# Performance work log

Measured on AMD Instinct MI355X. Metric: run time of the kernel, lower is better.

Reference implementation:

```python
import jax, jax.numpy as jnp
import numpy as np
from jax import lax

B, N = 8, 107136          # batch, anchors (248*216*2)
SCORE_THRESH = 0.05
PRE_MAX = 2048            # nms_pre_max_sizes[0]
POST_MAX = 128            # nms_post_max_sizes[0]
IOU_THRESH = 0.5
NUM_DIR_BINS = 2
DIR_OFFSET = 0.0
POST_CENTER_RANGE = np.array([0.0, -39.68, -5.0, 69.12, 39.68, 5.0], np.float32)


def setup_inputs() -> dict:
    key = jax.random.key(0)
    k1, k2, k3, k4, k5 = jax.random.split(key, 5)
    box_preds = jax.random.normal(k1, (B, N, 7), jnp.float32) * 0.3
    cls_preds = jax.random.normal(k2, (B, N, 2), jnp.float32) * 2.0
    dir_preds = jax.random.normal(k3, (B, N, 2), jnp.float32)
    # realistic KITTI car anchors: (x, y, z, w, l, h, r)
    xs = jax.random.uniform(k4, (B, N), jnp.float32, 0.0, 69.12)
    ys = jax.random.uniform(k5, (B, N), jnp.float32, -39.68, 39.68)
    zs = jnp.full((B, N), -1.0, jnp.float32)
    w = jnp.full((B, N), 1.6, jnp.float32)
    l = jnp.full((B, N), 3.9, jnp.float32)
    h = jnp.full((B, N), 1.56, jnp.float32)
    r = jnp.broadcast_to(jnp.where(jnp.arange(N) % 2 == 0, 0.0, np.pi / 2).astype(jnp.float32), (B, N))
    anchors = jnp.stack([xs, ys, zs, w, l, h, r], axis=-1)
    return {"box_preds": box_preds, "cls_preds": cls_preds, "dir_preds": dir_preds, "anchors": anchors}


def _decode(bp, an):
    # GroundBox3dCoder.decode_torch (second/pointpillars), code order (x,y,z,w,l,h,r)
    xa, ya, za, wa, la, ha, ra = [an[..., i] for i in range(7)]
    xt, yt, zt, wt, lt, ht, rt = [bp[..., i] for i in range(7)]
    za = za + ha * 0.5
    diag = jnp.sqrt(la * la + wa * wa)
    xg = xt * diag + xa
    yg = yt * diag + ya
    zg = zt * ha + za
    lg = jnp.exp(lt) * la
    wg = jnp.exp(wt) * wa
    hg = jnp.exp(ht) * ha
    rg = rt + ra
    zg = zg - hg * 0.5
    return jnp.stack([xg, yg, zg, wg, lg, hg, rg], axis=-1)


def _standup(boxes):
    # boxes: [K,7] decoded; rotated 2d rect -> axis-aligned standup box (x1,y1,x2,y2)
    x, y, w, l, r = boxes[:, 0], boxes[:, 1], boxes[:, 3], boxes[:, 4], boxes[:, 6]
    c, s = jnp.abs(jnp.cos(r)), jnp.abs(jnp.sin(r))
    hx = 0.5 * (w * c + l * s)
    hy = 0.5 * (w * s + l * c)
    return jnp.stack([x - hx, y - hy, x + hx, y + hy], axis=-1)


def _pairwise_iou(bb):
    # bb: [K,4] standup boxes
    x1, y1, x2, y2 = bb[:, 0], bb[:, 1], bb[:, 2], bb[:, 3]
    area = (x2 - x1) * (y2 - y1)
    ix = jnp.maximum(0.0, jnp.minimum(x2[:, None], x2[None, :]) - jnp.maximum(x1[:, None], x1[None, :]))
    iy = jnp.maximum(0.0, jnp.minimum(y2[:, None], y2[None, :]) - jnp.maximum(y1[:, None], y1[None, :]))
    inter = ix * iy
    return inter / jnp.maximum(area[:, None] + area[None, :] - inter, 1e-8)


def _greedy_nms(ious, valid):
    K = valid.shape[0]
    idxs = jnp.arange(K)
    def body(i, keep):
        sup = (ious[i] > IOU_THRESH) & (idxs > i) & keep[i]
        return keep & ~sup
    return lax.fori_loop(0, K, body, valid)


def _limit_period(val, offset, period):
    return val - jnp.floor(val / period + offset) * period


def _predict_one(boxes, scores, dir_labels):
    # boxes [N,7], scores [N], dir_labels [N] int32 (already sorted? no: raw)
    masked = jnp.where(scores >= SCORE_THRESH, scores, -jnp.inf)
    top_s, idx = lax.top_k(masked, PRE_MAX)           # sorted desc
    b = boxes[idx]                                    # [K,7]
    dl = dir_labels[idx]
    valid = jnp.isfinite(top_s)
    ious = _pairwise_iou(_standup(b))
    keep = _greedy_nms(lax.stop_gradient(ious), valid)
    kept = jnp.where(keep, top_s, -jnp.inf)
    sel_s, sel_i = lax.top_k(kept, POST_MAX)
    sel_b = b[sel_i]
    sel_dl = dl[sel_i].astype(sel_b.dtype)
    period = 2.0 * np.pi / NUM_DIR_BINS
    dir_rot = _limit_period(sel_b[:, 6] - DIR_OFFSET, 0.0, period)
    new_r = dir_rot + DIR_OFFSET + period * sel_dl
    sel_b = jnp.concatenate([sel_b[:, :6], new_r[:, None]], axis=-1)
    pcr = jnp.asarray(POST_CENTER_RANGE)
    in_range = jnp.all(sel_b[:, :3] >= pcr[:3], axis=1) & jnp.all(sel_b[:, :3] <= pcr[3:], axis=1)
    mask = jnp.isfinite(sel_s) & in_range
    out_s = jnp.where(mask, sel_s, 0.0)
    out_b = jnp.where(mask[:, None], sel_b, 0.0)
    labels = jnp.zeros((POST_MAX,), jnp.int32)  # single fg class -> label 0
    return out_b, out_s, labels, mask


def reference(box_preds, cls_preds, dir_preds, anchors):
    decoded = _decode(box_preds, anchors)                    # [B,N,7]
    scores = jax.nn.softmax(cls_preds, axis=-1)[..., 1]      # [B,N]
    dir_labels = jnp.argmax(dir_preds, axis=-1).astype(jnp.int32)
    return jax.vmap(_predict_one)(decoded, scores, dir_labels)
```

## Files before the change

kernel.cpp:

```cpp
#include <hip/hip_runtime.h>
#include <stdint.h>

#define NB 8
#define NN 107136
#define TOTAL (NB * NN)
#define NPAIR (NN / 2)
#define PRE 2048
#define POST 128
#define CAP 4096
#define HBINS 128
#define KEYBASE 0xBF00u
#define SCORE_TH 0.05f
#define SH_BPB 53

static constexpr size_t OFF_SCORES = 0;
static constexpr size_t SZ_SCORES  = (size_t)TOTAL * 4;
static constexpr size_t OFF_HIST   = OFF_SCORES + SZ_SCORES;
static constexpr size_t SZ_HIST    = (size_t)NB * HBINS * 4;
static constexpr size_t OFF_CNT    = OFF_HIST + SZ_HIST;
static constexpr size_t SZ_CNT     = (size_t)NB * 64 * 4;
static constexpr size_t OFF_T      = OFF_CNT + SZ_CNT;
static constexpr size_t OFF_CAND   = OFF_T + 256;
static constexpr size_t SZ_CAND    = (size_t)NB * CAP * 8;
static constexpr size_t OFF_SELS   = OFF_CAND + SZ_CAND;
static constexpr size_t OFF_SELI   = OFF_SELS + (size_t)NB * PRE * 4;
static constexpr size_t OFF_SELB   = OFF_SELI + (size_t)NB * PRE * 4;
static constexpr size_t OFF_SBB    = OFF_SELB + (size_t)NB * PRE * 7 * 4;
static constexpr size_t OFF_SAR    = OFF_SBB + (size_t)NB * PRE * 4 * 4;
static constexpr size_t OFF_MASK   = OFF_SAR + (size_t)NB * PRE * 4;
static constexpr size_t SZ_MASK    = (size_t)NB * PRE * 32 * 8;


__global__ void k_zero(uint32_t* p, int nwords) {
    int g = blockIdx.x * 256 + threadIdx.x;
    if (g < nwords) p[g] = 0u;
}

__global__ void __launch_bounds__(256) k_scoreshist(const float* __restrict__ cls,
                                                    float* __restrict__ scores,
                                                    uint32_t* __restrict__ hist) {
    int b = blockIdx.y;
    __shared__ uint32_t lh[HBINS];
    int t = threadIdx.x;
    if (t < HBINS) lh[t] = 0u;
    __syncthreads();
    const float4* cp = (const float4*)cls + (size_t)b * NPAIR;
    float2* sp = (float2*)scores + (size_t)b * NPAIR;
#pragma unroll
    for (int k = 0; k < 4; k++) {
        int p = blockIdx.x * 1024 + k * 256 + t;
        if (p < NPAIR) {
            float4 c = cp[p];
            float m0 = fmaxf(c.x, c.y);
            float s0 = __fdiv_rn(expf(__fsub_rn(c.y, m0)),
                                 __fadd_rn(expf(__fsub_rn(c.x, m0)), expf(__fsub_rn(c.y, m0))));
            float m1 = fmaxf(c.z, c.w);
            float s1 = __fdiv_rn(expf(__fsub_rn(c.w, m1)),
                                 __fadd_rn(expf(__fsub_rn(c.z, m1)), expf(__fsub_rn(c.w, m1))));
            sp[p] = make_float2(s0, s1);
            if (s0 >= 0.5f) {
                uint32_t bin = ((__float_as_uint(s0) >> 16) | 0x8000u) - KEYBASE;
                if (bin > 127u) bin = 127u;
                atomicAdd(&lh[bin], 1u);
            }
            if (s1 >= 0.5f) {
                uint32_t bin = ((__float_as_uint(s1) >> 16) | 0x8000u) - KEYBASE;
                if (bin > 127u) bin = 127u;
                atomicAdd(&lh[bin], 1u);
            }
        }
    }
    __syncthreads();
    if (t < HBINS && lh[t]) atomicAdd(&hist[b * HBINS + t], lh[t]);
}

__global__ void __launch_bounds__(64) k_findT(const uint32_t* __restrict__ hist,
                                              uint32_t* __restrict__ Tout) {
    int b = blockIdx.x, t = threadIdx.x;
    const uint32_t* h = hist + b * HBINS;
    uint32_t h0 = h[2 * t], h1 = h[2 * t + 1];
    uint32_t v = h0 + h1;
    for (int off = 1; off < 64; off <<= 1) {
        uint32_t u = __shfl_down(v, off);
        if (t + off >= 64) u = 0u;
        v += u;
    }
    uint32_t total = __shfl(v, 0);
    int c = -1;
    if (v - h0 >= PRE) c = 2 * t + 1;
    else if (v >= PRE) c = 2 * t;
    for (int off = 32; off > 0; off >>= 1) c = max(c, __shfl_xor(c, off));
    if (t == 0) Tout[b] = (total >= PRE && c >= 0) ? (KEYBASE + (uint32_t)c) : 0u;
}

__global__ void __launch_bounds__(256) k_compact(const float* __restrict__ scores,
                                                 const uint32_t* __restrict__ T,
                                                 uint32_t* __restrict__ counts,
                                                 uint64_t* __restrict__ cand) {
    int g2 = blockIdx.x * 256 + threadIdx.x;
    int lane = threadIdx.x & 63, wid = threadIdx.x >> 6;
    float2 sv = ((const float2*)scores)[g2];
    int e0 = 2 * g2;
    int b = e0 / NN;
    uint32_t Tb = T[b];
    uint32_t key0 = __float_as_uint(sv.x) | 0x80000000u;
    uint32_t key1 = __float_as_uint(sv.y) | 0x80000000u;
    bool p0 = (sv.x >= SCORE_TH) && ((key0 >> 16) >= Tb);
    bool p1 = (sv.y >= SCORE_TH) && ((key1 >> 16) >= Tb);
    uint64_t bal0 = __ballot(p0), bal1 = __ballot(p1);
    uint32_t n0 = (uint32_t)__popcll(bal0);
    uint32_t wcnt = n0 + (uint32_t)__popcll(bal1);
    uint64_t below = (lane == 63) ? ~0ull >> 1 : ((1ull << lane) - 1ull);
    below = (1ull << lane) - 1ull;
    uint32_t off0 = (uint32_t)__popcll(bal0 & below);
    uint32_t off1 = n0 + (uint32_t)__popcll(bal1 & below);
    __shared__ uint32_t lcnt[2];
    __shared__ uint32_t gbase[2];
    __shared__ uint32_t wbase[4];
    int b0 = (blockIdx.x * 512) / NN;
    if (threadIdx.x < 2) lcnt[threadIdx.x] = 0u;
    __syncthreads();
    if (lane == 0 && wcnt) wbase[wid] = atomicAdd(&lcnt[b - b0], wcnt);
    __syncthreads();
    if (threadIdx.x < 2 && lcnt[threadIdx.x])
        gbase[threadIdx.x] = atomicAdd(&counts[(size_t)(b0 + threadIdx.x) * 64], lcnt[threadIdx.x]);
    __syncthreads();
    if (p0 | p1) {
        uint32_t base = gbase[b - b0] + wbase[wid];
        if (p0) {
            uint32_t slot = base + off0;
            if (slot < CAP)
                cand[(size_t)b * CAP + slot] =
                    ((uint64_t)key0 << 32) | (uint64_t)(0xFFFFFFFFu - (uint32_t)(e0 - b * NN));
        }
        if (p1) {
            uint32_t slot = base + off1;
            if (slot < CAP)
                cand[(size_t)b * CAP + slot] =
                    ((uint64_t)key1 << 32) | (uint64_t)(0xFFFFFFFFu - (uint32_t)(e0 + 1 - b * NN));
        }
    }
}

__global__ void __launch_bounds__(256) k_rank_decode(
        const uint64_t* __restrict__ cand, const uint32_t* __restrict__ counts,
        const float* __restrict__ box_preds, const float* __restrict__ anchors,
        float* __restrict__ selS, uint32_t* __restrict__ selI,
        float* __restrict__ selB, float* __restrict__ selBB, float* __restrict__ selA) {
    int b = blockIdx.y;
    int i = blockIdx.x * 256 + threadIdx.x;
    int m = (int)counts[(size_t)b * 64]; if (m > CAP) m = CAP;
    const uint64_t* cb = cand + (size_t)b * CAP;
    uint64_t mykey = (i < m) ? cb[i] : 0ull;
    __shared__ uint64_t tile[512];
    int rank = 0;
    for (int base = 0; base < m; base += 512) {
        int nt = min(512, m - base);
        for (int j = threadIdx.x; j < nt; j += 256) tile[j] = cb[base + j];
        __syncthreads();
        if (i < m) {
            int j = 0;
            for (; j + 8 <= nt; j += 8) {
#pragma unroll
                for (int u = 0; u < 8; u++) rank += (tile[j + u] > mykey) ? 1 : 0;
            }
            for (; j < nt; j++) rank += (tile[j] > mykey) ? 1 : 0;
        }
        __syncthreads();
    }
    if (i >= m || rank >= PRE) return;
    size_t o = (size_t)b * PRE + rank;
    uint32_t key = (uint32_t)(mykey >> 32);
    uint32_t idx = 0xFFFFFFFFu - (uint32_t)(mykey & 0xFFFFFFFFull);
    float score = __uint_as_float(key & 0x7FFFFFFFu);
    const float* bp = box_preds + ((size_t)b * NN + idx) * 7;
    const float* an = anchors + ((size_t)b * NN + idx) * 7;
    float xa = an[0], ya = an[1], za = an[2], wa = an[3], la = an[4], ha = an[5], ra = an[6];
    float xt = bp[0], yt = bp[1], zt = bp[2], wt = bp[3], lt = bp[4], ht = bp[5], rt = bp[6];
    float za2  = __fadd_rn(za, __fmul_rn(ha, 0.5f));
    float diag = sqrtf(__fadd_rn(__fmul_rn(la, la), __fmul_rn(wa, wa)));
    float xg = __fadd_rn(__fmul_rn(xt, diag), xa);
    float yg = __fadd_rn(__fmul_rn(yt, diag), ya);
    float zg = __fadd_rn(__fmul_rn(zt, ha), za2);
    float lg = __fmul_rn(expf(lt), la);
    float wg = __fmul_rn(expf(wt), wa);
    float hg = __fmul_rn(expf(ht), ha);
    float rg = __fadd_rn(rt, ra);
    zg = __fsub_rn(zg, __fmul_rn(hg, 0.5f));
    selS[o] = score; selI[o] = idx;
    selB[o * 7 + 0] = xg; selB[o * 7 + 1] = yg; selB[o * 7 + 2] = zg;
    selB[o * 7 + 3] = wg; selB[o * 7 + 4] = lg; selB[o * 7 + 5] = hg;
    selB[o * 7 + 6] = rg;
    float cc = fabsf(cosf(rg)), ss = fabsf(sinf(rg));
    float hx = __fmul_rn(0.5f, __fadd_rn(__fmul_rn(wg, cc), __fmul_rn(lg, ss)));
    float hy = __fmul_rn(0.5f, __fadd_rn(__fmul_rn(wg, ss), __fmul_rn(lg, cc)));
    float x1 = __fsub_rn(xg, hx), y1 = __fsub_rn(yg, hy);
    float x2 = __fadd_rn(xg, hx), y2 = __fadd_rn(yg, hy);
    selBB[o * 4 + 0] = x1; selBB[o * 4 + 1] = y1;
    selBB[o * 4 + 2] = x2; selBB[o * 4 + 3] = y2;
    selA[o] = __fmul_rn(__fsub_rn(x2, x1), __fsub_rn(y2, y1));
}

__global__ void __launch_bounds__(256) k_iou(const float* __restrict__ selBB,
                                             const float* __restrict__ selA,
                                             uint64_t* __restrict__ maskrows) {
    int b = blockIdx.y;
    int r0 = blockIdx.x * 64;
    __shared__ float sx1[PRE], sy1[PRE], sx2[PRE], sy2[PRE], sar[PRE];
    int t = threadIdx.x;
    for (int i = t; i < PRE; i += 256) {
        const float* p = selBB + ((size_t)b * PRE + i) * 4;
        sx1[i] = p[0]; sy1[i] = p[1]; sx2[i] = p[2]; sy2[i] = p[3];
        sar[i] = selA[(size_t)b * PRE + i];
    }
    __syncthreads();
    int w  = t & 31;
    int rl = t >> 5;
    int jbase = w * 64;
    float rx1[8], ry1[8], rx2[8], ry2[8], rar[8];
    int rows[8];
#pragma unroll
    for (int p = 0; p < 8; p++) {
        int i = r0 + rl * 8 + p;
        rows[p] = i;
        rx1[p] = sx1[i]; ry1[p] = sy1[i]; rx2[p] = sx2[i]; ry2[p] = sy2[i]; rar[p] = sar[i];
    }
    uint64_t bits[8] = {0, 0, 0, 0, 0, 0, 0, 0};
    for (int jj = 0; jj < 64; jj++) {
        int j = jbase + ((jj + w) & 63);
        float xj1 = sx1[j], yj1 = sy1[j], xj2 = sx2[j], yj2 = sy2[j], aj = sar[j];
#pragma unroll
        for (int p = 0; p < 8; p++) {
            float ix = fmaxf(0.f, __fsub_rn(fminf(rx2[p], xj2), fmaxf(rx1[p], xj1)));
            float iy = fmaxf(0.f, __fsub_rn(fminf(ry2[p], yj2), fmaxf(ry1[p], yj1)));
            float inter = __fmul_rn(ix, iy);
            float den = fmaxf(__fsub_rn(__fadd_rn(rar[p], aj), inter), 1e-8f);
            float iou = __fdiv_rn(inter, den);
            if (iou > 0.5f && j > rows[p]) bits[p] |= (1ull << (j - jbase));
        }
    }
#pragma unroll
    for (int p = 0; p < 8; p++)
        maskrows[((size_t)b * PRE + rows[p]) * 32 + w] = bits[p];
}

__global__ void __launch_bounds__(128) k_nms_final(
        const uint64_t* __restrict__ maskrows, const float* __restrict__ selS,
        const uint32_t* __restrict__ selI, const float* __restrict__ selB,
        const uint32_t* __restrict__ counts, const float* __restrict__ dir_preds,
        float* __restrict__ out) {
    int b = blockIdx.x;
    __shared__ int keptIdx[POST];
    __shared__ int keptCount;
    int t = threadIdx.x;
    int Mv = (int)counts[(size_t)b * 64]; if (Mv > PRE) Mv = PRE;
    if (t < 64) {
        uint64_t removed = 0ull;
        int kc = 0;
        const uint64_t* mb = maskrows + (size_t)b * PRE * 32;
        uint64_t pre[8];
#pragma unroll
        for (int d = 0; d < 8; d++)
            pre[d] = (t < 32 && d < Mv) ? mb[(size_t)d * 32 + t] : 0ull;
        for (int i = 0; i < Mv && kc < POST; i++) {
            uint64_t mrow = pre[i & 7];
            int nf = i + 8;
            pre[i & 7] = (t < 32 && nf < Mv) ? mb[(size_t)nf * 32 + t] : 0ull;
            uint64_t rw = __shfl(removed, i >> 6);
            if (!((rw >> (i & 63)) & 1ull)) {
                if (t == 0) keptIdx[kc] = i;
                kc++;
                removed |= mrow;
            }
        }
        if (t == 0) keptCount = kc;
    }
    __syncthreads();
    int kc = keptCount;
    size_t ob = (size_t)b * POST + t;
    float box[7] = {0.f, 0.f, 0.f, 0.f, 0.f, 0.f, 0.f};
    float sc = 0.f, mk = 0.f;
    if (t < kc) {
        int i = keptIdx[t];
        size_t o = (size_t)b * PRE + i;
        float s = selS[o];
        uint32_t idx = selI[o];
        const float* bx = selB + o * 7;
        float d0 = dir_preds[((size_t)b * NN + idx) * 2 + 0];
        float d1 = dir_preds[((size_t)b * NN + idx) * 2 + 1];
        float label = (d1 > d0) ? 1.0f : 0.0f;
        const float period = 3.14159265358979323846f;
        float r = bx[6];
        float dir_rot = __fsub_rn(r, __fmul_rn(floorf(__fdiv_rn(r, period)), period));
        float nr = __fadd_rn(dir_rot, __fmul_rn(period, label));
        float x = bx[0], y = bx[1], z = bx[2];
        bool in_range = (x >= 0.0f) && (y >= -39.68f) && (z >= -5.0f) &&
                        (x <= 69.12f) && (y <= 39.68f) && (z <= 5.0f);
        if (in_range) {
            box[0] = x; box[1] = y; box[2] = z;
            box[3] = bx[3]; box[4] = bx[4]; box[5] = bx[5]; box[6] = nr;
            sc = s; mk = 1.f;
        }
    }
    float* out_b = out;
    float* out_s = out + 7168;
    float* out_l = out + 8192;
    float* out_m = out + 9216;
    for (int c = 0; c < 7; c++) out_b[ob * 7 + c] = box[c];
    out_s[ob] = sc;
    out_l[ob] = 0.f;
    out_m[ob] = mk;
}

extern "C" void kernel_launch(void* const* d_in, const int* in_sizes, int n_in,
                              void* d_out, int out_size, void* d_ws, size_t ws_size,
                              hipStream_t stream) {
    const float* box_preds = (const float*)d_in[0];
    const float* cls_preds = (const float*)d_in[1];
    const float* dir_preds = (const float*)d_in[2];
    const float* anchors   = (const float*)d_in[3];
    float* out = (float*)d_out;
    char* ws = (char*)d_ws;

    float*    scores = (float*)(ws + OFF_SCORES);
    uint32_t* hist   = (uint32_t*)(ws + OFF_HIST);
    uint32_t* counts = (uint32_t*)(ws + OFF_CNT);
    uint32_t* T      = (uint32_t*)(ws + OFF_T);
    uint64_t* cand   = (uint64_t*)(ws + OFF_CAND);
    float*    selS   = (float*)(ws + OFF_SELS);
    uint32_t* selI   = (uint32_t*)(ws + OFF_SELI);
    float*    selB   = (float*)(ws + OFF_SELB);
    float*    selBB  = (float*)(ws + OFF_SBB);
    float*    selA   = (float*)(ws + OFF_SAR);
    uint64_t* maskrows = (uint64_t*)(ws + OFF_MASK);

    int zwords = (int)((SZ_HIST + SZ_CNT + 256) / 4);
    k_zero<<<(zwords + 255) / 256, 256, 0, stream>>>(hist, zwords);

    dim3 gSH(SH_BPB, NB);
    k_scoreshist<<<gSH, 256, 0, stream>>>(cls_preds, scores, hist);
    k_findT<<<NB, 64, 0, stream>>>(hist, T);
    k_compact<<<TOTAL / 512, 256, 0, stream>>>(scores, T, counts, cand);
    dim3 gRank(CAP / 256, NB);
    k_rank_decode<<<gRank, 256, 0, stream>>>(cand, counts, box_preds, anchors,
                                             selS, selI, selB, selBB, selA);
    dim3 gIou(PRE / 64, NB);
    k_iou<<<gIou, 256, 0, stream>>>(selBB, selA, maskrows);
    k_nms_final<<<NB, 128, 0, stream>>>(maskrows, selS, selI, selB, counts,
                                        dir_preds, out);
}
```

Before: 222.2 us.

## Drop zero kernel, rewrite rank with ballot counting, halve IoU rows per block

The score histogram now writes per-block partial histograms that k_findT reduces, so the global atomics and the separate zeroing kernel go away. k_findT also resets the candidate count and clears the candidate buffer. The rank kernel exits early for empty blocks and counts larger keys with wave ballots over keys read straight from global memory, replacing the shared-tile pairwise loop. The IoU kernel processes 4 rows per thread instead of 8, doubling the grid, and replaces the divide with a multiply-compare, which can flip a decision when inter/den is right at 0.5 under rounding.

```diff
diff --git a/kernel.cpp b/kernel.cpp
--- a/kernel.cpp
+++ b/kernel.cpp
@@ -16,7 +16,7 @@
 static constexpr size_t OFF_SCORES = 0;
 static constexpr size_t SZ_SCORES  = (size_t)TOTAL * 4;
 static constexpr size_t OFF_HIST   = OFF_SCORES + SZ_SCORES;
-static constexpr size_t SZ_HIST    = (size_t)NB * HBINS * 4;
+static constexpr size_t SZ_HIST    = (size_t)NB * SH_BPB * HBINS * 4;
 static constexpr size_t OFF_CNT    = OFF_HIST + SZ_HIST;
 static constexpr size_t SZ_CNT     = (size_t)NB * 64 * 4;
 static constexpr size_t OFF_T      = OFF_CNT + SZ_CNT;
@@ -31,14 +31,9 @@
 static constexpr size_t SZ_MASK    = (size_t)NB * PRE * 32 * 8;
 
 
-__global__ void k_zero(uint32_t* p, int nwords) {
-    int g = blockIdx.x * 256 + threadIdx.x;
-    if (g < nwords) p[g] = 0u;
-}
-
 __global__ void __launch_bounds__(256) k_scoreshist(const float* __restrict__ cls,
                                                     float* __restrict__ scores,
-                                                    uint32_t* __restrict__ hist) {
+                                                    uint32_t* __restrict__ hp) {
     int b = blockIdx.y;
     __shared__ uint32_t lh[HBINS];
     int t = threadIdx.x;
@@ -71,26 +66,42 @@
         }
     }
     __syncthreads();
-    if (t < HBINS && lh[t]) atomicAdd(&hist[b * HBINS + t], lh[t]);
-}
-
-__global__ void __launch_bounds__(64) k_findT(const uint32_t* __restrict__ hist,
-                                              uint32_t* __restrict__ Tout) {
+    if (t < HBINS) hp[((size_t)b * SH_BPB + blockIdx.x) * HBINS + t] = lh[t];
+}
+
+__global__ void __launch_bounds__(256) k_findT(const uint32_t* __restrict__ hp,
+                                               uint32_t* __restrict__ Tout,
+                                               uint32_t* __restrict__ counts,
+                                               uint64_t* __restrict__ cand) {
     int b = blockIdx.x, t = threadIdx.x;
-    const uint32_t* h = hist + b * HBINS;
-    uint32_t h0 = h[2 * t], h1 = h[2 * t + 1];
-    uint32_t v = h0 + h1;
-    for (int off = 1; off < 64; off <<= 1) {
-        uint32_t u = __shfl_down(v, off);
-        if (t + off >= 64) u = 0u;
-        v += u;
-    }
-    uint32_t total = __shfl(v, 0);
-    int c = -1;
-    if (v - h0 >= PRE) c = 2 * t + 1;
-    else if (v >= PRE) c = 2 * t;
-    for (int off = 32; off > 0; off >>= 1) c = max(c, __shfl_xor(c, off));
-    if (t == 0) Tout[b] = (total >= PRE && c >= 0) ? (KEYBASE + (uint32_t)c) : 0u;
+    __shared__ uint32_t hbin[HBINS];
+    if (t < HBINS) {
+        uint32_t s = 0;
+        for (int sg = 0; sg < SH_BPB; sg++)
+            s += hp[((size_t)b * SH_BPB + sg) * HBINS + t];
+        hbin[t] = s;
+    }
+    __syncthreads();
+    if (t < 64) {
+        uint32_t h0 = hbin[2 * t], h1 = hbin[2 * t + 1];
+        uint32_t v = h0 + h1;
+        for (int off = 1; off < 64; off <<= 1) {
+            uint32_t u = __shfl_down(v, off);
+            if (t + off >= 64) u = 0u;
+            v += u;
+        }
+        uint32_t total = __shfl(v, 0);
+        int c = -1;
+        if (v - h0 >= PRE) c = 2 * t + 1;
+        else if (v >= PRE) c = 2 * t;
+        for (int off = 32; off > 0; off >>= 1) c = max(c, __shfl_xor(c, off));
+        if (t == 0) {
+            Tout[b] = (total >= PRE && c >= 0) ? (KEYBASE + (uint32_t)c) : 0u;
+            counts[(size_t)b * 64] = 0u;
+        }
+    }
+    uint64_t* cb = cand + (size_t)b * CAP;
+    for (int i = t; i < CAP; i += 256) cb[i] = 0ull;
 }
 
 __global__ void __launch_bounds__(256) k_compact(const float* __restrict__ scores,
@@ -110,8 +121,7 @@
     uint64_t bal0 = __ballot(p0), bal1 = __ballot(p1);
     uint32_t n0 = (uint32_t)__popcll(bal0);
     uint32_t wcnt = n0 + (uint32_t)__popcll(bal1);
-    uint64_t below = (lane == 63) ? ~0ull >> 1 : ((1ull << lane) - 1ull);
-    below = (1ull << lane) - 1ull;
+    uint64_t below = (1ull << lane) - 1ull;
     uint32_t off0 = (uint32_t)__popcll(bal0 & below);
     uint32_t off1 = n0 + (uint32_t)__popcll(bal1 & below);
     __shared__ uint32_t lcnt[2];
@@ -142,33 +152,50 @@
     }
 }
 
-__global__ void __launch_bounds__(256) k_rank_decode(
+__global__ void __launch_bounds__(256) k_rankdecode(
         const uint64_t* __restrict__ cand, const uint32_t* __restrict__ counts,
         const float* __restrict__ box_preds, const float* __restrict__ anchors,
         float* __restrict__ selS, uint32_t* __restrict__ selI,
         float* __restrict__ selB, float* __restrict__ selBB, float* __restrict__ selA) {
     int b = blockIdx.y;
-    int i = blockIdx.x * 256 + threadIdx.x;
+    int i0 = blockIdx.x * 256;
     int m = (int)counts[(size_t)b * 64]; if (m > CAP) m = CAP;
+    if (i0 >= m) return;
     const uint64_t* cb = cand + (size_t)b * CAP;
-    uint64_t mykey = (i < m) ? cb[i] : 0ull;
-    __shared__ uint64_t tile[512];
-    int rank = 0;
-    for (int base = 0; base < m; base += 512) {
-        int nt = min(512, m - base);
-        for (int j = threadIdx.x; j < nt; j += 256) tile[j] = cb[base + j];
-        __syncthreads();
-        if (i < m) {
-            int j = 0;
-            for (; j + 8 <= nt; j += 8) {
-#pragma unroll
-                for (int u = 0; u < 8; u++) rank += (tile[j + u] > mykey) ? 1 : 0;
+    __shared__ uint64_t shI[256];
+    __shared__ uint32_t rp[4][4][64];
+    int t = threadIdx.x;
+    int lane = t & 63, w = t >> 6;
+    shI[t] = cb[i0 + t];
+    __syncthreads();
+    int sweeps = (m + 2047) / 2048;
+#pragma unroll
+    for (int q = 0; q < 4; q++) {
+        uint32_t accq = 0;
+        for (int s = 0; s < sweeps; s++) {
+            int jb = s * 2048 + w * 512;
+            if (jb < m) {
+                int j0 = jb + lane * 8;
+                uint64_t jk[8];
+#pragma unroll
+                for (int u = 0; u < 8; u++) jk[u] = cb[j0 + u];
+                for (int il = 0; il < 64; il++) {
+                    uint64_t ik = shI[q * 64 + il];
+                    uint32_t p = 0;
+#pragma unroll
+                    for (int u = 0; u < 8; u++)
+                        p += (uint32_t)__popcll(__ballot(jk[u] > ik));
+                    if (lane == il) accq += p;
+                }
             }
-            for (; j < nt; j++) rank += (tile[j] > mykey) ? 1 : 0;
-        }
-        __syncthreads();
-    }
+        }
+        rp[w][q][lane] = accq;
+    }
+    __syncthreads();
+    int i = i0 + t;
+    uint32_t rank = rp[0][w][lane] + rp[1][w][lane] + rp[2][w][lane] + rp[3][w][lane];
     if (i >= m || rank >= PRE) return;
+    uint64_t mykey = shI[t];
     size_t o = (size_t)b * PRE + rank;
     uint32_t key = (uint32_t)(mykey >> 32);
     uint32_t idx = 0xFFFFFFFFu - (uint32_t)(mykey & 0xFFFFFFFFull);
@@ -205,7 +232,7 @@
                                              const float* __restrict__ selA,
                                              uint64_t* __restrict__ maskrows) {
     int b = blockIdx.y;
-    int r0 = blockIdx.x * 64;
+    int r0 = blockIdx.x * 32;
     __shared__ float sx1[PRE], sy1[PRE], sx2[PRE], sy2[PRE], sar[PRE];
     int t = threadIdx.x;
     for (int i = t; i < PRE; i += 256) {
@@ -217,30 +244,30 @@
     int w  = t & 31;
     int rl = t >> 5;
     int jbase = w * 64;
-    float rx1[8], ry1[8], rx2[8], ry2[8], rar[8];
-    int rows[8];
-#pragma unroll
-    for (int p = 0; p < 8; p++) {
-        int i = r0 + rl * 8 + p;
+    float rx1[4], ry1[4], rx2[4], ry2[4], rar[4];
+    int rows[4];
+#pragma unroll
+    for (int p = 0; p < 4; p++) {
+        int i = r0 + rl * 4 + p;
         rows[p] = i;
         rx1[p] = sx1[i]; ry1[p] = sy1[i]; rx2[p] = sx2[i]; ry2[p] = sy2[i]; rar[p] = sar[i];
     }
-    uint64_t bits[8] = {0, 0, 0, 0, 0, 0, 0, 0};
+    uint64_t bits[4] = {0, 0, 0, 0};
     for (int jj = 0; jj < 64; jj++) {
         int j = jbase + ((jj + w) & 63);
         float xj1 = sx1[j], yj1 = sy1[j], xj2 = sx2[j], yj2 = sy2[j], aj = sar[j];
 #pragma unroll
-        for (int p = 0; p < 8; p++) {
+        for (int p = 0; p < 4; p++) {
             float ix = fmaxf(0.f, __fsub_rn(fminf(rx2[p], xj2), fmaxf(rx1[p], xj1)));
             float iy = fmaxf(0.f, __fsub_rn(fminf(ry2[p], yj2), fmaxf(ry1[p], yj1)));
             float inter = __fmul_rn(ix, iy);
             float den = fmaxf(__fsub_rn(__fadd_rn(rar[p], aj), inter), 1e-8f);
-            float iou = __fdiv_rn(inter, den);
-            if (iou > 0.5f && j > rows[p]) bits[p] |= (1ull << (j - jbase));
-        }
-    }
-#pragma unroll
-    for (int p = 0; p < 8; p++)
+            if (inter > __fmul_rn(0.5f, den) && j > rows[p])
+                bits[p] |= (1ull << (j - jbase));
+        }
+    }
+#pragma unroll
+    for (int p = 0; p < 4; p++)
         maskrows[((size_t)b * PRE + rows[p]) * 32 + w] = bits[p];
 }
 
@@ -323,7 +350,7 @@
     char* ws = (char*)d_ws;
 
     float*    scores = (float*)(ws + OFF_SCORES);
-    uint32_t* hist   = (uint32_t*)(ws + OFF_HIST);
+    uint32_t* hp     = (uint32_t*)(ws + OFF_HIST);
     uint32_t* counts = (uint32_t*)(ws + OFF_CNT);
     uint32_t* T      = (uint32_t*)(ws + OFF_T);
     uint64_t* cand   = (uint64_t*)(ws + OFF_CAND);
@@ -334,17 +361,14 @@
     float*    selA   = (float*)(ws + OFF_SAR);
     uint64_t* maskrows = (uint64_t*)(ws + OFF_MASK);
 
-    int zwords = (int)((SZ_HIST + SZ_CNT + 256) / 4);
-    k_zero<<<(zwords + 255) / 256, 256, 0, stream>>>(hist, zwords);
-
     dim3 gSH(SH_BPB, NB);
-    k_scoreshist<<<gSH, 256, 0, stream>>>(cls_preds, scores, hist);
-    k_findT<<<NB, 64, 0, stream>>>(hist, T);
+    k_scoreshist<<<gSH, 256, 0, stream>>>(cls_preds, scores, hp);
+    k_findT<<<NB, 256, 0, stream>>>(hp, T, counts, cand);
     k_compact<<<TOTAL / 512, 256, 0, stream>>>(scores, T, counts, cand);
     dim3 gRank(CAP / 256, NB);
-    k_rank_decode<<<gRank, 256, 0, stream>>>(cand, counts, box_preds, anchors,
-                                             selS, selI, selB, selBB, selA);
-    dim3 gIou(PRE / 64, NB);
+    k_rankdecode<<<gRank, 256, 0, stream>>>(cand, counts, box_preds, anchors,
+                                            selS, selI, selB, selBB, selA);
+    dim3 gIou(PRE / 32, NB);
     k_iou<<<gIou, 256, 0, stream>>>(selBB, selA, maskrows);
     k_nms_final<<<NB, 128, 0, stream>>>(maskrows, selS, selI, selB, counts,
                                         dir_preds, out);
```

Result: faster. 214.4 us (-3.5%).

## Drop zero and threshold kernels, per-block histograms, direct-global ranking, smaller IoU tiles

Applied to the files above, without the earlier changes.

Removes the zeroing and threshold-finding launches. Each score block now writes its own partial histogram, and every compact wave re-reduces those partials to find the threshold itself. Ranking now reads candidates straight from global memory without shared-memory tiling and exits early for empty blocks. The IoU kernel handles 4 rows per thread with twice as many blocks and swaps the divide for a multiply-compare. This saves two launches and the atomics but repeats histogram reduction work in every wave, and the multiply-compare could change borderline IoU decisions.

```diff
diff --git a/kernel.cpp b/kernel.cpp
--- a/kernel.cpp
+++ b/kernel.cpp
@@ -16,11 +16,10 @@
 static constexpr size_t OFF_SCORES = 0;
 static constexpr size_t SZ_SCORES  = (size_t)TOTAL * 4;
 static constexpr size_t OFF_HIST   = OFF_SCORES + SZ_SCORES;
-static constexpr size_t SZ_HIST    = (size_t)NB * HBINS * 4;
+static constexpr size_t SZ_HIST    = (size_t)NB * SH_BPB * HBINS * 4;
 static constexpr size_t OFF_CNT    = OFF_HIST + SZ_HIST;
 static constexpr size_t SZ_CNT     = (size_t)NB * 64 * 4;
-static constexpr size_t OFF_T      = OFF_CNT + SZ_CNT;
-static constexpr size_t OFF_CAND   = OFF_T + 256;
+static constexpr size_t OFF_CAND   = OFF_CNT + SZ_CNT + 256;
 static constexpr size_t SZ_CAND    = (size_t)NB * CAP * 8;
 static constexpr size_t OFF_SELS   = OFF_CAND + SZ_CAND;
 static constexpr size_t OFF_SELI   = OFF_SELS + (size_t)NB * PRE * 4;
@@ -31,15 +30,12 @@
 static constexpr size_t SZ_MASK    = (size_t)NB * PRE * 32 * 8;
 
 
-__global__ void k_zero(uint32_t* p, int nwords) {
-    int g = blockIdx.x * 256 + threadIdx.x;
-    if (g < nwords) p[g] = 0u;
-}
-
 __global__ void __launch_bounds__(256) k_scoreshist(const float* __restrict__ cls,
                                                     float* __restrict__ scores,
-                                                    uint32_t* __restrict__ hist) {
+                                                    uint32_t* __restrict__ hp,
+                                                    uint32_t* __restrict__ counts) {
     int b = blockIdx.y;
+    if (blockIdx.x == 0 && threadIdx.x == 0) counts[(size_t)b * 64] = 0u;
     __shared__ uint32_t lh[HBINS];
     int t = threadIdx.x;
     if (t < HBINS) lh[t] = 0u;
@@ -71,38 +67,39 @@
         }
     }
     __syncthreads();
-    if (t < HBINS && lh[t]) atomicAdd(&hist[b * HBINS + t], lh[t]);
-}
-
-__global__ void __launch_bounds__(64) k_findT(const uint32_t* __restrict__ hist,
-                                              uint32_t* __restrict__ Tout) {
-    int b = blockIdx.x, t = threadIdx.x;
-    const uint32_t* h = hist + b * HBINS;
-    uint32_t h0 = h[2 * t], h1 = h[2 * t + 1];
-    uint32_t v = h0 + h1;
-    for (int off = 1; off < 64; off <<= 1) {
-        uint32_t u = __shfl_down(v, off);
-        if (t + off >= 64) u = 0u;
-        v += u;
-    }
-    uint32_t total = __shfl(v, 0);
-    int c = -1;
-    if (v - h0 >= PRE) c = 2 * t + 1;
-    else if (v >= PRE) c = 2 * t;
-    for (int off = 32; off > 0; off >>= 1) c = max(c, __shfl_xor(c, off));
-    if (t == 0) Tout[b] = (total >= PRE && c >= 0) ? (KEYBASE + (uint32_t)c) : 0u;
+    if (t < HBINS) hp[((size_t)b * SH_BPB + blockIdx.x) * HBINS + t] = lh[t];
 }
 
 __global__ void __launch_bounds__(256) k_compact(const float* __restrict__ scores,
-                                                 const uint32_t* __restrict__ T,
+                                                 const uint32_t* __restrict__ hp,
                                                  uint32_t* __restrict__ counts,
                                                  uint64_t* __restrict__ cand) {
     int g2 = blockIdx.x * 256 + threadIdx.x;
     int lane = threadIdx.x & 63, wid = threadIdx.x >> 6;
-    float2 sv = ((const float2*)scores)[g2];
     int e0 = 2 * g2;
     int b = e0 / NN;
-    uint32_t Tb = T[b];
+
+    uint32_t h0 = 0, h1 = 0;
+    const uint32_t* hb = hp + (size_t)b * SH_BPB * HBINS;
+#pragma unroll 4
+    for (int sg = 0; sg < SH_BPB; sg++) {
+        h0 += hb[sg * HBINS + 2 * lane];
+        h1 += hb[sg * HBINS + 2 * lane + 1];
+    }
+    uint32_t v = h0 + h1;
+    for (int off = 1; off < 64; off <<= 1) {
+        uint32_t u = __shfl_down(v, off);
+        if (lane + off >= 64) u = 0u;
+        v += u;
+    }
+    uint32_t total = __shfl(v, 0);
+    int c = -1;
+    if (v - h0 >= PRE) c = 2 * lane + 1;
+    else if (v >= PRE) c = 2 * lane;
+    for (int off = 32; off > 0; off >>= 1) c = max(c, __shfl_xor(c, off));
+    uint32_t Tb = (total >= PRE && c >= 0) ? (KEYBASE + (uint32_t)c) : 0u;
+
+    float2 sv = ((const float2*)scores)[g2];
     uint32_t key0 = __float_as_uint(sv.x) | 0x80000000u;
     uint32_t key1 = __float_as_uint(sv.y) | 0x80000000u;
     bool p0 = (sv.x >= SCORE_TH) && ((key0 >> 16) >= Tb);
@@ -110,8 +107,7 @@
     uint64_t bal0 = __ballot(p0), bal1 = __ballot(p1);
     uint32_t n0 = (uint32_t)__popcll(bal0);
     uint32_t wcnt = n0 + (uint32_t)__popcll(bal1);
-    uint64_t below = (lane == 63) ? ~0ull >> 1 : ((1ull << lane) - 1ull);
-    below = (1ull << lane) - 1ull;
+    uint64_t below = (1ull << lane) - 1ull;
     uint32_t off0 = (uint32_t)__popcll(bal0 & below);
     uint32_t off1 = n0 + (uint32_t)__popcll(bal1 & below);
     __shared__ uint32_t lcnt[2];
@@ -148,27 +144,23 @@
         float* __restrict__ selS, uint32_t* __restrict__ selI,
         float* __restrict__ selB, float* __restrict__ selBB, float* __restrict__ selA) {
     int b = blockIdx.y;
+    int m = (int)counts[(size_t)b * 64]; if (m > CAP) m = CAP;
+    if (blockIdx.x * 256 >= m) return;
     int i = blockIdx.x * 256 + threadIdx.x;
-    int m = (int)counts[(size_t)b * 64]; if (m > CAP) m = CAP;
     const uint64_t* cb = cand + (size_t)b * CAP;
-    uint64_t mykey = (i < m) ? cb[i] : 0ull;
-    __shared__ uint64_t tile[512];
-    int rank = 0;
-    for (int base = 0; base < m; base += 512) {
-        int nt = min(512, m - base);
-        for (int j = threadIdx.x; j < nt; j += 256) tile[j] = cb[base + j];
-        __syncthreads();
-        if (i < m) {
-            int j = 0;
-            for (; j + 8 <= nt; j += 8) {
-#pragma unroll
-                for (int u = 0; u < 8; u++) rank += (tile[j + u] > mykey) ? 1 : 0;
-            }
-            for (; j < nt; j++) rank += (tile[j] > mykey) ? 1 : 0;
-        }
-        __syncthreads();
-    }
+    uint64_t mykey = (i < m) ? cb[i] : ~0ull;
+    uint32_t rank = 0;
+    int j = 0;
+    for (; j + 8 <= m; j += 8) {
+#pragma unroll
+        for (int u = 0; u < 8; u++) {
+            uint64_t jk = cb[j + u];
+            rank += (jk > mykey) ? 1u : 0u;
+        }
+    }
+    for (; j < m; j++) rank += (cb[j] > mykey) ? 1u : 0u;
     if (i >= m || rank >= PRE) return;
+
     size_t o = (size_t)b * PRE + rank;
     uint32_t key = (uint32_t)(mykey >> 32);
     uint32_t idx = 0xFFFFFFFFu - (uint32_t)(mykey & 0xFFFFFFFFull);
@@ -205,7 +197,7 @@
                                              const float* __restrict__ selA,
                                              uint64_t* __restrict__ maskrows) {
     int b = blockIdx.y;
-    int r0 = blockIdx.x * 64;
+    int r0 = blockIdx.x * 32;
     __shared__ float sx1[PRE], sy1[PRE], sx2[PRE], sy2[PRE], sar[PRE];
     int t = threadIdx.x;
     for (int i = t; i < PRE; i += 256) {
@@ -217,30 +209,30 @@
     int w  = t & 31;
     int rl = t >> 5;
     int jbase = w * 64;
-    float rx1[8], ry1[8], rx2[8], ry2[8], rar[8];
-    int rows[8];
-#pragma unroll
-    for (int p = 0; p < 8; p++) {
-        int i = r0 + rl * 8 + p;
+    float rx1[4], ry1[4], rx2[4], ry2[4], rar[4];
+    int rows[4];
+#pragma unroll
+    for (int p = 0; p < 4; p++) {
+        int i = r0 + rl * 4 + p;
         rows[p] = i;
         rx1[p] = sx1[i]; ry1[p] = sy1[i]; rx2[p] = sx2[i]; ry2[p] = sy2[i]; rar[p] = sar[i];
     }
-    uint64_t bits[8] = {0, 0, 0, 0, 0, 0, 0, 0};
+    uint64_t bits[4] = {0, 0, 0, 0};
     for (int jj = 0; jj < 64; jj++) {
         int j = jbase + ((jj + w) & 63);
         float xj1 = sx1[j], yj1 = sy1[j], xj2 = sx2[j], yj2 = sy2[j], aj = sar[j];
 #pragma unroll
-        for (int p = 0; p < 8; p++) {
+        for (int p = 0; p < 4; p++) {
             float ix = fmaxf(0.f, __fsub_rn(fminf(rx2[p], xj2), fmaxf(rx1[p], xj1)));
             float iy = fmaxf(0.f, __fsub_rn(fminf(ry2[p], yj2), fmaxf(ry1[p], yj1)));
             float inter = __fmul_rn(ix, iy);
             float den = fmaxf(__fsub_rn(__fadd_rn(rar[p], aj), inter), 1e-8f);
-            float iou = __fdiv_rn(inter, den);
-            if (iou > 0.5f && j > rows[p]) bits[p] |= (1ull << (j - jbase));
-        }
-    }
-#pragma unroll
-    for (int p = 0; p < 8; p++)
+            if (inter > __fmul_rn(0.5f, den) && j > rows[p])
+                bits[p] |= (1ull << (j - jbase));
+        }
+    }
+#pragma unroll
+    for (int p = 0; p < 4; p++)
         maskrows[((size_t)b * PRE + rows[p]) * 32 + w] = bits[p];
 }
 
@@ -323,9 +315,8 @@
     char* ws = (char*)d_ws;
 
     float*    scores = (float*)(ws + OFF_SCORES);
-    uint32_t* hist   = (uint32_t*)(ws + OFF_HIST);
+    uint32_t* hp     = (uint32_t*)(ws + OFF_HIST);
     uint32_t* counts = (uint32_t*)(ws + OFF_CNT);
-    uint32_t* T      = (uint32_t*)(ws + OFF_T);
     uint64_t* cand   = (uint64_t*)(ws + OFF_CAND);
     float*    selS   = (float*)(ws + OFF_SELS);
     uint32_t* selI   = (uint32_t*)(ws + OFF_SELI);
@@ -334,17 +325,13 @@
     float*    selA   = (float*)(ws + OFF_SAR);
     uint64_t* maskrows = (uint64_t*)(ws + OFF_MASK);
 
-    int zwords = (int)((SZ_HIST + SZ_CNT + 256) / 4);
-    k_zero<<<(zwords + 255) / 256, 256, 0, stream>>>(hist, zwords);
-
     dim3 gSH(SH_BPB, NB);
-    k_scoreshist<<<gSH, 256, 0, stream>>>(cls_preds, scores, hist);
-    k_findT<<<NB, 64, 0, stream>>>(hist, T);
-    k_compact<<<TOTAL / 512, 256, 0, stream>>>(scores, T, counts, cand);
+    k_scoreshist<<<gSH, 256, 0, stream>>>(cls_preds, scores, hp, counts);
+    k_compact<<<TOTAL / 512, 256, 0, stream>>>(scores, hp, counts, cand);
     dim3 gRank(CAP / 256, NB);
     k_rank_decode<<<gRank, 256, 0, stream>>>(cand, counts, box_preds, anchors,
                                              selS, selI, selB, selBB, selA);
-    dim3 gIou(PRE / 64, NB);
+    dim3 gIou(PRE / 32, NB);
     k_iou<<<gIou, 256, 0, stream>>>(selBB, selA, maskrows);
     k_nms_final<<<NB, 128, 0, stream>>>(maskrows, selS, selI, selB, counts,
                                         dir_preds, out);
```

After: 274.2 us. +23.4%, slower.
